# Kernel optimization log

Measured on AMD Instinct MI355X. Metric: run time of the kernel, lower is better.

The kernel has to match this reference:

```python
import jax, jax.numpy as jnp
import numpy as np

B, S, H, DH = 1, 4096, 8, 40  # hardcoded in the original forward
D = H * DH  # 320

def setup_inputs() -> dict:
    key = jax.random.key(0)
    ks = jax.random.split(key, 6)
    s = 1.0 / np.sqrt(D)
    return {
        "x": jax.random.normal(ks[0], (B, S, D), dtype=jnp.float32),
        "Wq": jax.random.normal(ks[1], (D, D), dtype=jnp.float32) * s,
        "Wk": jax.random.normal(ks[2], (D, D), dtype=jnp.float32) * s,
        "Wv": jax.random.normal(ks[3], (D, D), dtype=jnp.float32) * s,
        "Wo": jax.random.normal(ks[4], (D, D), dtype=jnp.float32) * s,
        "bo": jnp.zeros((D,), dtype=jnp.float32),
    }

def reference(x, Wq, Wk, Wv, Wo, bo):
    scale = DH ** (-0.5)
    # nn.Linear(bias=False): y = x @ W^T. context = x (self-attention).
    q = x @ Wq.T
    k = x @ Wk.T
    v = x @ Wv.T
    # split heads: [B,S,D] -> [B*H, S, DH]
    def split_heads(t):
        return t.reshape(B, S, H, DH).transpose(0, 2, 1, 3).reshape(B * H, S, DH)
    q, k, v = split_heads(q), split_heads(k), split_heads(v)
    # fp32 QK^T (original forces float), softmax, AV
    sim = jnp.einsum('bid,bjd->bij', q.astype(jnp.float32), k.astype(jnp.float32)) * scale
    attn = jax.nn.softmax(sim, axis=-1)
    out = jnp.einsum('bij,bjd->bid', attn, v)
    # merge heads: [B*H, S, DH] -> [B, S, D]
    out = out.reshape(B, H, S, DH).transpose(0, 2, 1, 3).reshape(B, S, D)
    return out @ Wo.T + bo
```

## Files before the change

### kernel.cpp

```cpp
#include <hip/hip_runtime.h>
#include <math.h>


#define NS 4096
#define ND 320
#define SCALE2 0.2281101152f
#define HS48 196608
#define VTH 163840
#define XN 1310720

typedef __attribute__((ext_vector_type(8))) short bf16x8;
typedef __attribute__((ext_vector_type(16))) float f32x16;

static __device__ __forceinline__ unsigned short f2bru(float f) {
  return (unsigned short)((__builtin_bit_cast(unsigned int, f) + 0x8000u) >> 16);
}
static __device__ __forceinline__ unsigned int pk2ru(float a, float b) {
  unsigned int ua = __builtin_bit_cast(unsigned int, a) + 0x8000u;
  unsigned int ub = __builtin_bit_cast(unsigned int, b) + 0x8000u;
  return __builtin_amdgcn_perm(ub, ua, 0x07060302u);
}
static __device__ __forceinline__ unsigned int pk2t(float a, float b) {
  return __builtin_amdgcn_perm(__builtin_bit_cast(unsigned int, b),
                               __builtin_bit_cast(unsigned int, a), 0x07060302u);
}
static __device__ __forceinline__ float fexp2(float x) {
  return __builtin_amdgcn_exp2f(x);
}
static __device__ __forceinline__ bf16x8 ld8(const unsigned short* p) {
  union { uint2 u[2]; bf16x8 v; } c;
  c.u[0] = *(const uint2*)p;
  c.u[1] = *(const uint2*)(p + 4);
  return c.v;
}
static __device__ __forceinline__ uint4 ld16u(const unsigned short* p) {
  uint2 a = *(const uint2*)p, b = *(const uint2*)(p + 4);
  return make_uint4(a.x, a.y, b.x, b.y);
}
static __device__ __forceinline__ void st16(unsigned short* p, uint4 v) {
  *(uint2*)p = make_uint2(v.x, v.y);
  *(uint2*)(p + 4) = make_uint2(v.z, v.w);
}
static __device__ __forceinline__ int sig32(int q) {
  int s = q >> 4, h2 = (q >> 3) & 1, j = q & 7;
  return (s << 4) | ((j >> 2) << 3) | (h2 << 2) | (j & 3);
}

__global__ __launch_bounds__(256) void proj_qkv_kernel(
    const float* __restrict__ x, const float* __restrict__ Wq,
    const float* __restrict__ Wk, const float* __restrict__ Wv,
    unsigned short* __restrict__ Qp, unsigned short* __restrict__ Kp,
    unsigned short* __restrict__ Vt) {
  const int zi = blockIdx.y;
  const int z = zi / 5;
  const int bnn = (zi - z * 5) * 64;
  const float* W = (z == 0) ? Wq : (z == 1) ? Wk : Wv;
  __shared__ __align__(16) unsigned short As[128 * 76];
  __shared__ __align__(16) unsigned short Bs[64 * 76];
  const int t = threadIdx.x;
  const int w = t >> 6, l = t & 63, l31 = l & 31, hi = l >> 5;
  const int bm = blockIdx.x * 128;
  const int m0 = w * 32;
  f32x16 acc0 = {0,0,0,0,0,0,0,0,0,0,0,0,0,0,0,0};
  f32x16 acc1 = {0,0,0,0,0,0,0,0,0,0,0,0,0,0,0,0};
  const unsigned short* af = As + (m0 + l31) * 76 + hi * 8;
  const unsigned short* bf0 = Bs + l31 * 76 + hi * 8;
  const unsigned short* bf1 = Bs + (32 + l31) * 76 + hi * 8;
  for (int k0 = 0; k0 < ND; k0 += 64) {
    __syncthreads();
#pragma unroll
    for (int i = 0; i < 4; i++) {
      int c = t + i * 256;
      int row = c >> 3, kc = (c & 7) << 3;
      const float* g = x + (bm + row) * ND + k0 + kc;
      float4 v0 = *(const float4*)g, v1 = *(const float4*)(g + 4);
      st16(As + row * 76 + kc,
           make_uint4(pk2ru(v0.x, v0.y), pk2ru(v0.z, v0.w),
                      pk2ru(v1.x, v1.y), pk2ru(v1.z, v1.w)));
    }
#pragma unroll
    for (int i = 0; i < 2; i++) {
      int c = t + i * 256;
      int row = c >> 3, kc = (c & 7) << 3;
      const float* g = W + (bnn + row) * ND + k0 + kc;
      float4 v0 = *(const float4*)g, v1 = *(const float4*)(g + 4);
      st16(Bs + row * 76 + kc,
           make_uint4(pk2ru(v0.x, v0.y), pk2ru(v0.z, v0.w),
                      pk2ru(v1.x, v1.y), pk2ru(v1.z, v1.w)));
    }
    __syncthreads();
#pragma unroll
    for (int ks = 0; ks < 4; ks++) {
      bf16x8 A = ld8(af + ks * 16);
      acc0 = __builtin_amdgcn_mfma_f32_32x32x16_bf16(A, ld8(bf0 + ks * 16), acc0, 0, 0, 0);
      acc1 = __builtin_amdgcn_mfma_f32_32x32x16_bf16(A, ld8(bf1 + ks * 16), acc1, 0, 0, 0);
    }
  }
  __syncthreads();
  if (z < 2) {
    unsigned short* Tile = As;
    unsigned short* Y = (z == 0) ? Qp : Kp;
    const float sc = (z == 0) ? SCALE2 : 1.0f;
    const unsigned int padw = (z == 0) ? 0xC200u : 0x3F80u;
#pragma unroll
    for (int r2 = 0; r2 < 16; r2++) {
      int lr = m0 + (r2 & 3) + 8 * (r2 >> 2) + 4 * hi;
      Tile[lr * 68 + l31] = f2bru(acc0[r2] * sc);
      Tile[lr * 68 + 32 + l31] = f2bru(acc1[r2] * sc);
    }
    __syncthreads();
#pragma unroll
    for (int i = 0; i < 4; i++) {
      int c = t + i * 256;
      int row = c >> 3, ch = c & 7;
      int j = bnn + ch * 8;
      int h = j / 40, dh = j - h * 40;
      uint4 v = ld16u(Tile + row * 68 + ch * 8);
      st16(Y + h * HS48 + (bm + row) * 48 + dh, v);
      if (dh == 0)
        st16(Y + h * HS48 + (bm + row) * 48 + 40, make_uint4(padw, 0u, 0u, 0u));
    }
  } else {
    unsigned short* Tile = As;
#pragma unroll
    for (int r2 = 0; r2 < 16; r2++) {
      int lr = m0 + (r2 & 3) + 8 * (r2 >> 2) + 4 * hi;
      Tile[l31 * 132 + lr] = f2bru(acc0[r2]);
      Tile[(32 + l31) * 132 + lr] = f2bru(acc1[r2]);
    }
    __syncthreads();
#pragma unroll
    for (int i = 0; i < 4; i++) {
      int c = t + i * 256;
      int row = c >> 4, ch = c & 15;
      int j = bnn + row;
      int h = j / 40, dd = j - h * 40;
      uint4 v = ld16u(Tile + row * 132 + ch * 8);
      st16(Vt + h * VTH + dd * NS + bm + ch * 8, v);
    }
  }
}

__global__ __launch_bounds__(256, 4) void attn_kernel(
    const unsigned short* __restrict__ Qp, const unsigned short* __restrict__ Kp,
    const unsigned short* __restrict__ Vt, unsigned short* __restrict__ Op,
    float* __restrict__ Lp) {
  const int b = blockIdx.x;
  const int h = b & 7, ks = (b >> 3) & 3, qt = b >> 5;
  const int t = threadIdx.x;
  const int w = t >> 6, l = t & 63, l31 = l & 31, hi = l >> 5;
  __shared__ __align__(16) unsigned short Lds[16384];
  for (int i = t; i < 544; i += 256) {
    int bsel = (i >= 272) ? 1 : 0;
    int ui = i - bsel * 272;
    ((unsigned int*)(Lds + bsel * 8192 + 4352 + 40 * 68))[ui] =
        (ui < 34) ? 0x3F803F80u : 0u;
  }

  const int kbase = ks * 1024;
  const int qbase = qt * 128 + w * 32;
  const unsigned short* qp = Qp + h * HS48 + (qbase + l31) * 48 + hi * 8;
  bf16x8 qf0 = *(const bf16x8*)qp;
  bf16x8 qf1 = *(const bf16x8*)(qp + 16);
  bf16x8 qf2 = *(const bf16x8*)(qp + 32);

  const f32x16 Z = {0,0,0,0,0,0,0,0,0,0,0,0,0,0,0,0};
  f32x16 oa0 = Z, oa1 = Z;

  const int id1 = t + 256;
  const bool has2 = (t < 192);
  const int kr0 = t / 6, kc0 = t - kr0 * 6;
  const unsigned short* g0 = Kp + h * HS48 + (kbase + kr0) * 48 + kc0 * 8;
  const int w0 = ((kr0 & 32) | sig32(kr0 & 31)) * 68 + kc0 * 8;
  const unsigned short* g1;
  int w1, inc1;
  if (id1 < 384) {
    int kr = id1 / 6, kc = id1 - kr * 6;
    g1 = Kp + h * HS48 + (kbase + kr) * 48 + kc * 8;
    w1 = ((kr & 32) | sig32(kr & 31)) * 68 + kc * 8;
    inc1 = 64 * 48;
  } else {
    int vid = id1 - 384, vr = vid >> 3, vc = vid & 7;
    g1 = Vt + h * VTH + vr * NS + kbase + vc * 8;
    w1 = 4352 + vr * 68 + vc * 8;
    inc1 = 64;
  }
  const int vid2 = t + 128;
  const int vr2 = vid2 >> 3, vc2 = vid2 & 7;
  const unsigned short* g2 = Vt + h * VTH + vr2 * NS + kbase + vc2 * 8;
  const int w2 = 4352 + vr2 * 68 + vc2 * 8;

  const int rk  = l31 * 68 + hi * 8;
  const int rv0 = 4352 + l31 * 68 + hi * 8;
  const int rv1 = 4352 + (32 + (l31 & 15)) * 68 + hi * 8;

  uint4 r0 = *(const uint4*)g0; g0 += 3072;
  uint4 r1 = *(const uint4*)g1; g1 += inc1;
  uint4 r2{};
  if (has2) { r2 = *(const uint4*)g2; g2 += 64; }
  st16(Lds + w0, r0);
  st16(Lds + w1, r1);
  if (has2) st16(Lds + w2, r2);
  r0 = *(const uint4*)g0; g0 += 3072;
  r1 = *(const uint4*)g1; g1 += inc1;
  if (has2) { r2 = *(const uint4*)g2; g2 += 64; }
  __syncthreads();

  for (int it = 0; it < 16; ++it) {
    const int bo = (it & 1) << 13;
    const int bn = bo ^ 8192;
    st16(Lds + bn + w0, r0);
    st16(Lds + bn + w1, r1);
    if (has2) st16(Lds + bn + w2, r2);
    r0 = *(const uint4*)g0; g0 += 3072;
    r1 = *(const uint4*)g1; g1 += inc1;
    if (has2) { r2 = *(const uint4*)g2; g2 += 64; }

    const unsigned short* kf0 = Lds + bo + rk;
    const unsigned short* kf1 = kf0 + 2176;
    const unsigned short* vf0 = Lds + bo + rv0;
    const unsigned short* vf1 = Lds + bo + rv1;

    {
      f32x16 s0 = __builtin_amdgcn_mfma_f32_32x32x16_bf16(ld8(kf0), qf0, Z, 0, 0, 0);
      s0 = __builtin_amdgcn_mfma_f32_32x32x16_bf16(ld8(kf0 + 16), qf1, s0, 0, 0, 0);
      s0 = __builtin_amdgcn_mfma_f32_32x32x16_bf16(ld8(kf0 + 32), qf2, s0, 0, 0, 0);
      unsigned int pw[8];
#pragma unroll
      for (int i = 0; i < 8; i++)
        pw[i] = pk2t(fexp2(s0[2 * i]), fexp2(s0[2 * i + 1]));
      bf16x8 pf0 = __builtin_bit_cast(bf16x8, make_uint4(pw[0], pw[1], pw[2], pw[3]));
      bf16x8 pf1 = __builtin_bit_cast(bf16x8, make_uint4(pw[4], pw[5], pw[6], pw[7]));
      oa0 = __builtin_amdgcn_mfma_f32_32x32x16_bf16(pf0, ld8(vf0), oa0, 0, 0, 0);
      oa1 = __builtin_amdgcn_mfma_f32_32x32x16_bf16(pf0, ld8(vf1), oa1, 0, 0, 0);
      oa0 = __builtin_amdgcn_mfma_f32_32x32x16_bf16(pf1, ld8(vf0 + 16), oa0, 0, 0, 0);
      oa1 = __builtin_amdgcn_mfma_f32_32x32x16_bf16(pf1, ld8(vf1 + 16), oa1, 0, 0, 0);
    }
    {
      f32x16 s1 = __builtin_amdgcn_mfma_f32_32x32x16_bf16(ld8(kf1), qf0, Z, 0, 0, 0);
      s1 = __builtin_amdgcn_mfma_f32_32x32x16_bf16(ld8(kf1 + 16), qf1, s1, 0, 0, 0);
      s1 = __builtin_amdgcn_mfma_f32_32x32x16_bf16(ld8(kf1 + 32), qf2, s1, 0, 0, 0);
      unsigned int pw[8];
#pragma unroll
      for (int i = 0; i < 8; i++)
        pw[i] = pk2t(fexp2(s1[2 * i]), fexp2(s1[2 * i + 1]));
      bf16x8 pf2 = __builtin_bit_cast(bf16x8, make_uint4(pw[0], pw[1], pw[2], pw[3]));
      bf16x8 pf3 = __builtin_bit_cast(bf16x8, make_uint4(pw[4], pw[5], pw[6], pw[7]));
      oa0 = __builtin_amdgcn_mfma_f32_32x32x16_bf16(pf2, ld8(vf0 + 32), oa0, 0, 0, 0);
      oa1 = __builtin_amdgcn_mfma_f32_32x32x16_bf16(pf2, ld8(vf1 + 32), oa1, 0, 0, 0);
      oa0 = __builtin_amdgcn_mfma_f32_32x32x16_bf16(pf3, ld8(vf0 + 48), oa0, 0, 0, 0);
      oa1 = __builtin_amdgcn_mfma_f32_32x32x16_bf16(pf3, ld8(vf1 + 48), oa1, 0, 0, 0);
    }
    __syncthreads();
  }

  unsigned short* opb = Op + ks * XN + h * 163840;
  float* lpb = Lp + ks * 32768 + h * NS;
#pragma unroll
  for (int r2i = 0; r2i < 16; r2i++) {
    int qr = qbase + (r2i & 3) + 8 * (r2i >> 2) + 4 * hi;
    opb[qr * 40 + l31] = f2bru(oa0[r2i]);
    if (l31 < 8) opb[qr * 40 + 32 + l31] = f2bru(oa1[r2i]);
    if (l31 == 8) lpb[qr] = oa1[r2i];
  }
}

__global__ __launch_bounds__(256) void combine_kernel(
    const unsigned short* __restrict__ Op, const float* __restrict__ Lp,
    unsigned short* __restrict__ Xo) {
  int e = (blockIdx.x * 256 + threadIdx.x) * 2;
  int h = e / 163840;
  int r = e - h * 163840;
  int s = r / 40;
  int dh = r - s * 40;
  float a0 = 0.f, a1 = 0.f, lsum = 0.f;
#pragma unroll
  for (int k = 0; k < 4; k++) {
    unsigned int u = *(const unsigned int*)(Op + k * XN + e);
    a0 += __builtin_bit_cast(float, u << 16);
    a1 += __builtin_bit_cast(float, u & 0xFFFF0000u);
    lsum += Lp[k * 32768 + h * NS + s];
  }
  float inv = 1.0f / lsum;
  *(unsigned int*)(Xo + s * ND + h * 40 + dh) = pk2ru(a0 * inv, a1 * inv);
}

__global__ __launch_bounds__(256) void proj_out_kernel(
    const unsigned short* __restrict__ Xo, const float* __restrict__ Wo,
    const float* __restrict__ bo, float* __restrict__ out) {
  __shared__ __align__(16) unsigned short As[128 * 76];
  __shared__ __align__(16) unsigned short Bs[64 * 76];
  const int t = threadIdx.x;
  const int w = t >> 6, l = t & 63, l31 = l & 31, hi = l >> 5;
  const int bm = blockIdx.x * 128;
  const int bnn = blockIdx.y * 64;
  const int m0 = w * 32;
  f32x16 acc0 = {0,0,0,0,0,0,0,0,0,0,0,0,0,0,0,0};
  f32x16 acc1 = {0,0,0,0,0,0,0,0,0,0,0,0,0,0,0,0};
  const unsigned short* af = As + (m0 + l31) * 76 + hi * 8;
  const unsigned short* bf0 = Bs + l31 * 76 + hi * 8;
  const unsigned short* bf1 = Bs + (32 + l31) * 76 + hi * 8;
  for (int k0 = 0; k0 < ND; k0 += 64) {
    __syncthreads();
#pragma unroll
    for (int i = 0; i < 4; i++) {
      int c = t + i * 256;
      int row = c >> 3, kc = (c & 7) << 3;
      uint4 v = *(const uint4*)(Xo + (bm + row) * ND + k0 + kc);
      st16(As + row * 76 + kc, v);
    }
#pragma unroll
    for (int i = 0; i < 2; i++) {
      int c = t + i * 256;
      int row = c >> 3, kc = (c & 7) << 3;
      const float* g = Wo + (bnn + row) * ND + k0 + kc;
      float4 v0 = *(const float4*)g, v1 = *(const float4*)(g + 4);
      st16(Bs + row * 76 + kc,
           make_uint4(pk2ru(v0.x, v0.y), pk2ru(v0.z, v0.w),
                      pk2ru(v1.x, v1.y), pk2ru(v1.z, v1.w)));
    }
    __syncthreads();
#pragma unroll
    for (int ks = 0; ks < 4; ks++) {
      bf16x8 A = ld8(af + ks * 16);
      acc0 = __builtin_amdgcn_mfma_f32_32x32x16_bf16(A, ld8(bf0 + ks * 16), acc0, 0, 0, 0);
      acc1 = __builtin_amdgcn_mfma_f32_32x32x16_bf16(A, ld8(bf1 + ks * 16), acc1, 0, 0, 0);
    }
  }
  const int j0 = bnn + l31, j1 = bnn + 32 + l31;
  const float bj0 = bo[j0], bj1 = bo[j1];
#pragma unroll
  for (int r2 = 0; r2 < 16; r2++) {
    int row = bm + m0 + (r2 & 3) + 8 * (r2 >> 2) + 4 * hi;
    out[row * ND + j0] = acc0[r2] + bj0;
    out[row * ND + j1] = acc1[r2] + bj1;
  }
}

extern "C" void kernel_launch(void* const* d_in, const int* in_sizes, int n_in,
                              void* d_out, int out_size, void* d_ws, size_t ws_size,
                              hipStream_t stream) {
  (void)in_sizes; (void)n_in; (void)out_size; (void)ws_size;
  const float* x  = (const float*)d_in[0];
  const float* Wq = (const float*)d_in[1];
  const float* Wk = (const float*)d_in[2];
  const float* Wv = (const float*)d_in[3];
  const float* Wo = (const float*)d_in[4];
  const float* bo = (const float*)d_in[5];
  float* out = (float*)d_out;

  unsigned short* Qp = (unsigned short*)d_ws;
  unsigned short* Kp = Qp + 8 * HS48;
  unsigned short* Vt = Kp + 8 * HS48;
  unsigned short* Xo = Vt + 8 * VTH;
  unsigned short* Op = Xo + XN;
  float* Lp = (float*)(Op + 4 * XN);

  proj_qkv_kernel<<<dim3(32, 15), 256, 0, stream>>>(x, Wq, Wk, Wv, Qp, Kp, Vt);
  attn_kernel<<<dim3(1024), 256, 0, stream>>>(Qp, Kp, Vt, Op, Lp);
  combine_kernel<<<dim3(2560), 256, 0, stream>>>(Op, Lp, Xo);
  proj_out_kernel<<<dim3(32, 5), 256, 0, stream>>>(Xo, Wo, bo, out);
}
```

Measured before the change: 120.7 us.

## Fuse split-K combine into output projection and pad LDS for 128-bit accesses

Removes the separate combine kernel by having the output-projection GEMM read the four split-K partial outputs and row sums, normalize them, and convert to bf16 while loading its A tile. LDS row strides change (76→88 in GEMMs; 56/72 for K/V in attention) so 16-byte aligned ds_read/write_b128 can replace paired 8-byte accesses. This saves a launch and one intermediate round trip through global memory. In exchange, the output projection now reads the partials redundantly across its 5 column blocks and recomputes the row sums.

```diff
diff --git a/kernel.cpp b/kernel.cpp
--- a/kernel.cpp
+++ b/kernel.cpp
@@ -9,6 +9,11 @@
 #define VTH 163840
 #define XN 1310720
 
+#define KSTR 56
+#define VSTR 72
+#define VB   3584
+#define BUF  7040
+
 typedef __attribute__((ext_vector_type(8))) short bf16x8;
 typedef __attribute__((ext_vector_type(16))) float f32x16;
 
@@ -27,11 +32,11 @@
 static __device__ __forceinline__ float fexp2(float x) {
   return __builtin_amdgcn_exp2f(x);
 }
-static __device__ __forceinline__ bf16x8 ld8(const unsigned short* p) {
-  union { uint2 u[2]; bf16x8 v; } c;
-  c.u[0] = *(const uint2*)p;
-  c.u[1] = *(const uint2*)(p + 4);
-  return c.v;
+static __device__ __forceinline__ bf16x8 ld8a(const unsigned short* p) {
+  return __builtin_bit_cast(bf16x8, *(const uint4*)p);
+}
+static __device__ __forceinline__ void st16a(unsigned short* p, uint4 v) {
+  *(uint4*)p = v;
 }
 static __device__ __forceinline__ uint4 ld16u(const unsigned short* p) {
   uint2 a = *(const uint2*)p, b = *(const uint2*)(p + 4);
@@ -55,17 +60,17 @@
   const int z = zi / 5;
   const int bnn = (zi - z * 5) * 64;
   const float* W = (z == 0) ? Wq : (z == 1) ? Wk : Wv;
-  __shared__ __align__(16) unsigned short As[128 * 76];
-  __shared__ __align__(16) unsigned short Bs[64 * 76];
+  __shared__ __align__(16) unsigned short As[128 * 88];
+  __shared__ __align__(16) unsigned short Bs[64 * 88];
   const int t = threadIdx.x;
   const int w = t >> 6, l = t & 63, l31 = l & 31, hi = l >> 5;
   const int bm = blockIdx.x * 128;
   const int m0 = w * 32;
   f32x16 acc0 = {0,0,0,0,0,0,0,0,0,0,0,0,0,0,0,0};
   f32x16 acc1 = {0,0,0,0,0,0,0,0,0,0,0,0,0,0,0,0};
-  const unsigned short* af = As + (m0 + l31) * 76 + hi * 8;
-  const unsigned short* bf0 = Bs + l31 * 76 + hi * 8;
-  const unsigned short* bf1 = Bs + (32 + l31) * 76 + hi * 8;
+  const unsigned short* af = As + (m0 + l31) * 88 + hi * 8;
+  const unsigned short* bf0 = Bs + l31 * 88 + hi * 8;
+  const unsigned short* bf1 = Bs + (32 + l31) * 88 + hi * 8;
   for (int k0 = 0; k0 < ND; k0 += 64) {
     __syncthreads();
 #pragma unroll
@@ -74,9 +79,9 @@
       int row = c >> 3, kc = (c & 7) << 3;
       const float* g = x + (bm + row) * ND + k0 + kc;
       float4 v0 = *(const float4*)g, v1 = *(const float4*)(g + 4);
-      st16(As + row * 76 + kc,
-           make_uint4(pk2ru(v0.x, v0.y), pk2ru(v0.z, v0.w),
-                      pk2ru(v1.x, v1.y), pk2ru(v1.z, v1.w)));
+      st16a(As + row * 88 + kc,
+            make_uint4(pk2ru(v0.x, v0.y), pk2ru(v0.z, v0.w),
+                       pk2ru(v1.x, v1.y), pk2ru(v1.z, v1.w)));
     }
 #pragma unroll
     for (int i = 0; i < 2; i++) {
@@ -84,16 +89,16 @@
       int row = c >> 3, kc = (c & 7) << 3;
       const float* g = W + (bnn + row) * ND + k0 + kc;
       float4 v0 = *(const float4*)g, v1 = *(const float4*)(g + 4);
-      st16(Bs + row * 76 + kc,
-           make_uint4(pk2ru(v0.x, v0.y), pk2ru(v0.z, v0.w),
-                      pk2ru(v1.x, v1.y), pk2ru(v1.z, v1.w)));
+      st16a(Bs + row * 88 + kc,
+            make_uint4(pk2ru(v0.x, v0.y), pk2ru(v0.z, v0.w),
+                       pk2ru(v1.x, v1.y), pk2ru(v1.z, v1.w)));
     }
     __syncthreads();
 #pragma unroll
     for (int ks = 0; ks < 4; ks++) {
-      bf16x8 A = ld8(af + ks * 16);
-      acc0 = __builtin_amdgcn_mfma_f32_32x32x16_bf16(A, ld8(bf0 + ks * 16), acc0, 0, 0, 0);
-      acc1 = __builtin_amdgcn_mfma_f32_32x32x16_bf16(A, ld8(bf1 + ks * 16), acc1, 0, 0, 0);
+      bf16x8 A = ld8a(af + ks * 16);
+      acc0 = __builtin_amdgcn_mfma_f32_32x32x16_bf16(A, ld8a(bf0 + ks * 16), acc0, 0, 0, 0);
+      acc1 = __builtin_amdgcn_mfma_f32_32x32x16_bf16(A, ld8a(bf1 + ks * 16), acc1, 0, 0, 0);
     }
   }
   __syncthreads();
@@ -149,12 +154,13 @@
   const int h = b & 7, ks = (b >> 3) & 3, qt = b >> 5;
   const int t = threadIdx.x;
   const int w = t >> 6, l = t & 63, l31 = l & 31, hi = l >> 5;
-  __shared__ __align__(16) unsigned short Lds[16384];
-  for (int i = t; i < 544; i += 256) {
-    int bsel = (i >= 272) ? 1 : 0;
-    int ui = i - bsel * 272;
-    ((unsigned int*)(Lds + bsel * 8192 + 4352 + 40 * 68))[ui] =
-        (ui < 34) ? 0x3F803F80u : 0u;
+  __shared__ __align__(16) unsigned short Lds[2 * BUF];
+  for (int i = t; i < 576; i += 256) {
+    int bsel = (i >= 288) ? 1 : 0;
+    int ui = i - bsel * 288;
+    int rr = ui / 36, cc = ui - rr * 36;
+    ((unsigned int*)Lds)[bsel * (BUF / 2) + (VB / 2) + (40 + rr) * 36 + cc] =
+        (rr == 0 && cc < 32) ? 0x3F803F80u : 0u;
   }
 
   const int kbase = ks * 1024;
@@ -171,85 +177,85 @@
   const bool has2 = (t < 192);
   const int kr0 = t / 6, kc0 = t - kr0 * 6;
   const unsigned short* g0 = Kp + h * HS48 + (kbase + kr0) * 48 + kc0 * 8;
-  const int w0 = ((kr0 & 32) | sig32(kr0 & 31)) * 68 + kc0 * 8;
+  const int w0 = ((kr0 & 32) | sig32(kr0 & 31)) * KSTR + kc0 * 8;
   const unsigned short* g1;
   int w1, inc1;
   if (id1 < 384) {
     int kr = id1 / 6, kc = id1 - kr * 6;
     g1 = Kp + h * HS48 + (kbase + kr) * 48 + kc * 8;
-    w1 = ((kr & 32) | sig32(kr & 31)) * 68 + kc * 8;
+    w1 = ((kr & 32) | sig32(kr & 31)) * KSTR + kc * 8;
     inc1 = 64 * 48;
   } else {
     int vid = id1 - 384, vr = vid >> 3, vc = vid & 7;
     g1 = Vt + h * VTH + vr * NS + kbase + vc * 8;
-    w1 = 4352 + vr * 68 + vc * 8;
+    w1 = VB + vr * VSTR + vc * 8;
     inc1 = 64;
   }
   const int vid2 = t + 128;
   const int vr2 = vid2 >> 3, vc2 = vid2 & 7;
   const unsigned short* g2 = Vt + h * VTH + vr2 * NS + kbase + vc2 * 8;
-  const int w2 = 4352 + vr2 * 68 + vc2 * 8;
-
-  const int rk  = l31 * 68 + hi * 8;
-  const int rv0 = 4352 + l31 * 68 + hi * 8;
-  const int rv1 = 4352 + (32 + (l31 & 15)) * 68 + hi * 8;
+  const int w2 = VB + vr2 * VSTR + vc2 * 8;
+
+  const int rk  = l31 * KSTR + hi * 8;
+  const int rv0 = VB + l31 * VSTR + hi * 8;
+  const int rv1 = VB + (32 + (l31 & 15)) * VSTR + hi * 8;
 
   uint4 r0 = *(const uint4*)g0; g0 += 3072;
   uint4 r1 = *(const uint4*)g1; g1 += inc1;
   uint4 r2{};
   if (has2) { r2 = *(const uint4*)g2; g2 += 64; }
-  st16(Lds + w0, r0);
-  st16(Lds + w1, r1);
-  if (has2) st16(Lds + w2, r2);
+  st16a(Lds + w0, r0);
+  st16a(Lds + w1, r1);
+  if (has2) st16a(Lds + w2, r2);
   r0 = *(const uint4*)g0; g0 += 3072;
   r1 = *(const uint4*)g1; g1 += inc1;
   if (has2) { r2 = *(const uint4*)g2; g2 += 64; }
   __syncthreads();
 
   for (int it = 0; it < 16; ++it) {
-    const int bo = (it & 1) << 13;
-    const int bn = bo ^ 8192;
-    st16(Lds + bn + w0, r0);
-    st16(Lds + bn + w1, r1);
-    if (has2) st16(Lds + bn + w2, r2);
+    const int bo = (it & 1) ? BUF : 0;
+    const int bn = BUF - bo;
+    st16a(Lds + bn + w0, r0);
+    st16a(Lds + bn + w1, r1);
+    if (has2) st16a(Lds + bn + w2, r2);
     r0 = *(const uint4*)g0; g0 += 3072;
     r1 = *(const uint4*)g1; g1 += inc1;
     if (has2) { r2 = *(const uint4*)g2; g2 += 64; }
 
     const unsigned short* kf0 = Lds + bo + rk;
-    const unsigned short* kf1 = kf0 + 2176;
+    const unsigned short* kf1 = kf0 + 32 * KSTR;
     const unsigned short* vf0 = Lds + bo + rv0;
     const unsigned short* vf1 = Lds + bo + rv1;
 
     {
-      f32x16 s0 = __builtin_amdgcn_mfma_f32_32x32x16_bf16(ld8(kf0), qf0, Z, 0, 0, 0);
-      s0 = __builtin_amdgcn_mfma_f32_32x32x16_bf16(ld8(kf0 + 16), qf1, s0, 0, 0, 0);
-      s0 = __builtin_amdgcn_mfma_f32_32x32x16_bf16(ld8(kf0 + 32), qf2, s0, 0, 0, 0);
+      f32x16 s0 = __builtin_amdgcn_mfma_f32_32x32x16_bf16(ld8a(kf0), qf0, Z, 0, 0, 0);
+      s0 = __builtin_amdgcn_mfma_f32_32x32x16_bf16(ld8a(kf0 + 16), qf1, s0, 0, 0, 0);
+      s0 = __builtin_amdgcn_mfma_f32_32x32x16_bf16(ld8a(kf0 + 32), qf2, s0, 0, 0, 0);
       unsigned int pw[8];
 #pragma unroll
       for (int i = 0; i < 8; i++)
         pw[i] = pk2t(fexp2(s0[2 * i]), fexp2(s0[2 * i + 1]));
       bf16x8 pf0 = __builtin_bit_cast(bf16x8, make_uint4(pw[0], pw[1], pw[2], pw[3]));
       bf16x8 pf1 = __builtin_bit_cast(bf16x8, make_uint4(pw[4], pw[5], pw[6], pw[7]));
-      oa0 = __builtin_amdgcn_mfma_f32_32x32x16_bf16(pf0, ld8(vf0), oa0, 0, 0, 0);
-      oa1 = __builtin_amdgcn_mfma_f32_32x32x16_bf16(pf0, ld8(vf1), oa1, 0, 0, 0);
-      oa0 = __builtin_amdgcn_mfma_f32_32x32x16_bf16(pf1, ld8(vf0 + 16), oa0, 0, 0, 0);
-      oa1 = __builtin_amdgcn_mfma_f32_32x32x16_bf16(pf1, ld8(vf1 + 16), oa1, 0, 0, 0);
+      oa0 = __builtin_amdgcn_mfma_f32_32x32x16_bf16(pf0, ld8a(vf0), oa0, 0, 0, 0);
+      oa1 = __builtin_amdgcn_mfma_f32_32x32x16_bf16(pf0, ld8a(vf1), oa1, 0, 0, 0);
+      oa0 = __builtin_amdgcn_mfma_f32_32x32x16_bf16(pf1, ld8a(vf0 + 16), oa0, 0, 0, 0);
+      oa1 = __builtin_amdgcn_mfma_f32_32x32x16_bf16(pf1, ld8a(vf1 + 16), oa1, 0, 0, 0);
     }
     {
-      f32x16 s1 = __builtin_amdgcn_mfma_f32_32x32x16_bf16(ld8(kf1), qf0, Z, 0, 0, 0);
-      s1 = __builtin_amdgcn_mfma_f32_32x32x16_bf16(ld8(kf1 + 16), qf1, s1, 0, 0, 0);
-      s1 = __builtin_amdgcn_mfma_f32_32x32x16_bf16(ld8(kf1 + 32), qf2, s1, 0, 0, 0);
+      f32x16 s1 = __builtin_amdgcn_mfma_f32_32x32x16_bf16(ld8a(kf1), qf0, Z, 0, 0, 0);
+      s1 = __builtin_amdgcn_mfma_f32_32x32x16_bf16(ld8a(kf1 + 16), qf1, s1, 0, 0, 0);
+      s1 = __builtin_amdgcn_mfma_f32_32x32x16_bf16(ld8a(kf1 + 32), qf2, s1, 0, 0, 0);
       unsigned int pw[8];
 #pragma unroll
       for (int i = 0; i < 8; i++)
         pw[i] = pk2t(fexp2(s1[2 * i]), fexp2(s1[2 * i + 1]));
       bf16x8 pf2 = __builtin_bit_cast(bf16x8, make_uint4(pw[0], pw[1], pw[2], pw[3]));
       bf16x8 pf3 = __builtin_bit_cast(bf16x8, make_uint4(pw[4], pw[5], pw[6], pw[7]));
-      oa0 = __builtin_amdgcn_mfma_f32_32x32x16_bf16(pf2, ld8(vf0 + 32), oa0, 0, 0, 0);
-      oa1 = __builtin_amdgcn_mfma_f32_32x32x16_bf16(pf2, ld8(vf1 + 32), oa1, 0, 0, 0);
-      oa0 = __builtin_amdgcn_mfma_f32_32x32x16_bf16(pf3, ld8(vf0 + 48), oa0, 0, 0, 0);
-      oa1 = __builtin_amdgcn_mfma_f32_32x32x16_bf16(pf3, ld8(vf1 + 48), oa1, 0, 0, 0);
+      oa0 = __builtin_amdgcn_mfma_f32_32x32x16_bf16(pf2, ld8a(vf0 + 32), oa0, 0, 0, 0);
+      oa1 = __builtin_amdgcn_mfma_f32_32x32x16_bf16(pf2, ld8a(vf1 + 32), oa1, 0, 0, 0);
+      oa0 = __builtin_amdgcn_mfma_f32_32x32x16_bf16(pf3, ld8a(vf0 + 48), oa0, 0, 0, 0);
+      oa1 = __builtin_amdgcn_mfma_f32_32x32x16_bf16(pf3, ld8a(vf1 + 48), oa1, 0, 0, 0);
     }
     __syncthreads();
   }
@@ -265,31 +271,12 @@
   }
 }
 
-__global__ __launch_bounds__(256) void combine_kernel(
+__global__ __launch_bounds__(256) void proj_out_kernel(
     const unsigned short* __restrict__ Op, const float* __restrict__ Lp,
-    unsigned short* __restrict__ Xo) {
-  int e = (blockIdx.x * 256 + threadIdx.x) * 2;
-  int h = e / 163840;
-  int r = e - h * 163840;
-  int s = r / 40;
-  int dh = r - s * 40;
-  float a0 = 0.f, a1 = 0.f, lsum = 0.f;
-#pragma unroll
-  for (int k = 0; k < 4; k++) {
-    unsigned int u = *(const unsigned int*)(Op + k * XN + e);
-    a0 += __builtin_bit_cast(float, u << 16);
-    a1 += __builtin_bit_cast(float, u & 0xFFFF0000u);
-    lsum += Lp[k * 32768 + h * NS + s];
-  }
-  float inv = 1.0f / lsum;
-  *(unsigned int*)(Xo + s * ND + h * 40 + dh) = pk2ru(a0 * inv, a1 * inv);
-}
-
-__global__ __launch_bounds__(256) void proj_out_kernel(
-    const unsigned short* __restrict__ Xo, const float* __restrict__ Wo,
-    const float* __restrict__ bo, float* __restrict__ out) {
-  __shared__ __align__(16) unsigned short As[128 * 76];
-  __shared__ __align__(16) unsigned short Bs[64 * 76];
+    const float* __restrict__ Wo, const float* __restrict__ bo,
+    float* __restrict__ out) {
+  __shared__ __align__(16) unsigned short As[128 * 88];
+  __shared__ __align__(16) unsigned short Bs[64 * 88];
   const int t = threadIdx.x;
   const int w = t >> 6, l = t & 63, l31 = l & 31, hi = l >> 5;
   const int bm = blockIdx.x * 128;
@@ -297,17 +284,39 @@
   const int m0 = w * 32;
   f32x16 acc0 = {0,0,0,0,0,0,0,0,0,0,0,0,0,0,0,0};
   f32x16 acc1 = {0,0,0,0,0,0,0,0,0,0,0,0,0,0,0,0};
-  const unsigned short* af = As + (m0 + l31) * 76 + hi * 8;
-  const unsigned short* bf0 = Bs + l31 * 76 + hi * 8;
-  const unsigned short* bf1 = Bs + (32 + l31) * 76 + hi * 8;
+  const unsigned short* af = As + (m0 + l31) * 88 + hi * 8;
+  const unsigned short* bf0 = Bs + l31 * 88 + hi * 8;
+  const unsigned short* bf1 = Bs + (32 + l31) * 88 + hi * 8;
   for (int k0 = 0; k0 < ND; k0 += 64) {
     __syncthreads();
 #pragma unroll
     for (int i = 0; i < 4; i++) {
       int c = t + i * 256;
-      int row = c >> 3, kc = (c & 7) << 3;
-      uint4 v = *(const uint4*)(Xo + (bm + row) * ND + k0 + kc);
-      st16(As + row * 76 + kc, v);
+      int row = c >> 3, kc = c & 7;
+      int k = k0 + kc * 8;
+      int hh = k / 40, dh = k - hh * 40;
+      int s = bm + row;
+      const unsigned short* src = Op + hh * 163840 + s * 40 + dh;
+      float ls = Lp[hh * NS + s] + Lp[32768 + hh * NS + s] +
+                 Lp[65536 + hh * NS + s] + Lp[98304 + hh * NS + s];
+      float inv = 1.0f / ls;
+      float a0 = 0.f, a1 = 0.f, a2 = 0.f, a3 = 0.f;
+      float a4 = 0.f, a5 = 0.f, a6 = 0.f, a7 = 0.f;
+#pragma unroll
+      for (int p = 0; p < 4; p++) {
+        uint4 u = *(const uint4*)(src + p * XN);
+        a0 += __builtin_bit_cast(float, u.x << 16);
+        a1 += __builtin_bit_cast(float, u.x & 0xFFFF0000u);
+        a2 += __builtin_bit_cast(float, u.y << 16);
+        a3 += __builtin_bit_cast(float, u.y & 0xFFFF0000u);
+        a4 += __builtin_bit_cast(float, u.z << 16);
+        a5 += __builtin_bit_cast(float, u.z & 0xFFFF0000u);
+        a6 += __builtin_bit_cast(float, u.w << 16);
+        a7 += __builtin_bit_cast(float, u.w & 0xFFFF0000u);
+      }
+      st16a(As + row * 88 + kc * 8,
+            make_uint4(pk2ru(a0 * inv, a1 * inv), pk2ru(a2 * inv, a3 * inv),
+                       pk2ru(a4 * inv, a5 * inv), pk2ru(a6 * inv, a7 * inv)));
     }
 #pragma unroll
     for (int i = 0; i < 2; i++) {
@@ -315,16 +324,16 @@
       int row = c >> 3, kc = (c & 7) << 3;
       const float* g = Wo + (bnn + row) * ND + k0 + kc;
       float4 v0 = *(const float4*)g, v1 = *(const float4*)(g + 4);
-      st16(Bs + row * 76 + kc,
-           make_uint4(pk2ru(v0.x, v0.y), pk2ru(v0.z, v0.w),
-                      pk2ru(v1.x, v1.y), pk2ru(v1.z, v1.w)));
+      st16a(Bs + row * 88 + kc,
+            make_uint4(pk2ru(v0.x, v0.y), pk2ru(v0.z, v0.w),
+                       pk2ru(v1.x, v1.y), pk2ru(v1.z, v1.w)));
     }
     __syncthreads();
 #pragma unroll
     for (int ks = 0; ks < 4; ks++) {
-      bf16x8 A = ld8(af + ks * 16);
-      acc0 = __builtin_amdgcn_mfma_f32_32x32x16_bf16(A, ld8(bf0 + ks * 16), acc0, 0, 0, 0);
-      acc1 = __builtin_amdgcn_mfma_f32_32x32x16_bf16(A, ld8(bf1 + ks * 16), acc1, 0, 0, 0);
+      bf16x8 A = ld8a(af + ks * 16);
+      acc0 = __builtin_amdgcn_mfma_f32_32x32x16_bf16(A, ld8a(bf0 + ks * 16), acc0, 0, 0, 0);
+      acc1 = __builtin_amdgcn_mfma_f32_32x32x16_bf16(A, ld8a(bf1 + ks * 16), acc1, 0, 0, 0);
     }
   }
   const int j0 = bnn + l31, j1 = bnn + 32 + l31;
@@ -352,12 +361,10 @@
   unsigned short* Qp = (unsigned short*)d_ws;
   unsigned short* Kp = Qp + 8 * HS48;
   unsigned short* Vt = Kp + 8 * HS48;
-  unsigned short* Xo = Vt + 8 * VTH;
-  unsigned short* Op = Xo + XN;
+  unsigned short* Op = Vt + 8 * VTH;
   float* Lp = (float*)(Op + 4 * XN);
 
   proj_qkv_kernel<<<dim3(32, 15), 256, 0, stream>>>(x, Wq, Wk, Wv, Qp, Kp, Vt);
   attn_kernel<<<dim3(1024), 256, 0, stream>>>(Qp, Kp, Vt, Op, Lp);
-  combine_kernel<<<dim3(2560), 256, 0, stream>>>(Op, Lp, Xo);
-  proj_out_kernel<<<dim3(32, 5), 256, 0, stream>>>(Xo, Wo, bo, out);
-}
+  proj_out_kernel<<<dim3(32, 5), 256, 0, stream>>>(Op, Lp, Wo, bo, out);
+}
```

Measured after the change: 156.7 us. 29.8% more time.
